# Performance work log

Measured on AMD Instinct MI355X. Metric: run time of the kernel, lower is better.

Reference implementation:

```python
import jax, jax.numpy as jnp
import numpy as np

N, E = 50000, 200000          # nodes, edges
S, V = 256, 128               # 256x0e scalars, 128x1o vectors -> node dim 640
EDGE_DIM, HID = 64, 256
NUM_ATOM, NUM_BOND = 16, 5
FAN_TP = S * S + V * V        # fully-connected TP fan-in for rescale


def setup_inputs() -> dict:
    key = jax.random.key(0)
    ks = jax.random.split(key, 12)
    h_final = jax.random.normal(ks[0], (N, S + 3 * V), dtype=jnp.float32)
    e_final = jax.random.normal(ks[1], (E, EDGE_DIM), dtype=jnp.float32)
    target_node_mask = jnp.ones((N,), dtype=bool)
    target_edge_mask = jnp.ones((E,), dtype=bool)
    edge_index = jax.random.randint(ks[2], (2, E), 0, N)

    def lin(k, o, i):
        return (jax.random.normal(k, (o, i), jnp.float32) / np.sqrt(i)).astype(jnp.float32)

    return {
        "h_final": h_final,
        "e_final": e_final,
        "target_node_mask": target_node_mask,
        "target_edge_mask": target_edge_mask,
        "edge_index": edge_index,
        "Ws_w": lin(ks[3], S, S),          # LinearRS on scalar irreps (with bias)
        "Ws_b": jnp.zeros((S,), jnp.float32),
        "Wv": lin(ks[4], V, V),            # LinearRS on 1o irreps (no bias)
        "Wcoord": (jax.random.normal(ks[5], (V,), jnp.float32) / np.sqrt(V)),  # 128x1o -> 1x1o
        "W_tp00": jax.random.normal(ks[6], (S, S), jnp.float32),  # 0e x 0e -> 0e path weights
        "W_tp11": jax.random.normal(ks[7], (V, V), jnp.float32),  # 1o x 1o -> 0e path weights
        "atom_W1": lin(ks[8], HID, S), "atom_b1": jnp.zeros((HID,), jnp.float32),
        "atom_W2": lin(ks[9], NUM_ATOM, HID), "atom_b2": jnp.zeros((NUM_ATOM,), jnp.float32),
        "bond_W1": lin(ks[10], HID, 1 + EDGE_DIM), "bond_b1": jnp.zeros((HID,), jnp.float32),
        "bond_W2": lin(ks[11], NUM_BOND, HID), "bond_b2": jnp.zeros((NUM_BOND,), jnp.float32),
    }


def reference(h_final, e_final, target_node_mask, target_edge_mask, edge_index,
              Ws_w, Ws_b, Wv, Wcoord, W_tp00, W_tp11,
              atom_W1, atom_b1, atom_W2, atom_b2,
              bond_W1, bond_b1, bond_W2, bond_b2):
    # --- node heads (masks are all-True here; boolean gather kept for faithfulness) ---
    x = h_final[target_node_mask]                 # [Nt, 640]
    xs = x[:, :S]                                 # scalar (0e) part [Nt, 256]
    xv = x[:, S:].reshape(-1, V, 3)               # vector (1o) part [Nt, 128, 3]

    scalar_feats = xs @ Ws_w.T + Ws_b             # node_scalar_proj (LinearRS)
    atom_type_logits = jax.nn.silu(scalar_feats @ atom_W1.T + atom_b1) @ atom_W2.T + atom_b2

    vec = jnp.einsum('nci,dc->ndi', xv, Wv)       # node_vector_proj, per-component channel mix
    predicted_r0 = jnp.einsum('nci,c->ni', vec, Wcoord)  # coord_head -> [Nt, 3]

    # --- bond head: edge gather + fully-connected tensor product to 0e ---
    ei = edge_index[:, target_edge_mask]
    row, col = ei[0], ei[1]
    hr, hc = h_final[row], h_final[col]           # [Et, 640] each
    sr, sc = hr[:, :S], hc[:, :S]
    vr = hr[:, S:].reshape(-1, V, 3)
    vc = hc[:, S:].reshape(-1, V, 3)
    # paths: 0e(x)0e->0e and 1o(x)1o->0e (dot product, CG norm 1/sqrt(3)), rescaled by fan-in
    tp = (jnp.einsum('ei,ej,ij->e', sr, sc, W_tp00)
          + jnp.einsum('eci,edi,cd->e', vr, vc, W_tp11) / np.sqrt(3.0)) / np.sqrt(FAN_TP)
    bond_in = jnp.concatenate([tp[:, None], e_final[target_edge_mask]], axis=-1)  # [Et, 65]
    bond_logits = jax.nn.silu(bond_in @ bond_W1.T + bond_b1) @ bond_W2.T + bond_b2

    return atom_type_logits, predicted_r0, bond_logits
```

## Files before the change

kernel.cpp:

```cpp
#include <hip/hip_runtime.h>

typedef unsigned short u16;
typedef unsigned int u32;
typedef float f32x4 __attribute__((ext_vector_type(4)));
typedef float f32x2 __attribute__((ext_vector_type(2)));
typedef short s16x8 __attribute__((ext_vector_type(8)));
typedef __bf16 bf16x8 __attribute__((ext_vector_type(8)));

#define NNODE 50000
#define NEDGE 200000
#define INV_SQRT3 0.57735026918962576f
#define INV_SQRT_FAN 0.0034938562148434216f

__device__ inline float b2f(u16 x) {
    unsigned u = ((unsigned)x) << 16;
    return __builtin_bit_cast(float, u);
}
__device__ inline u16 f2b(float f) {
    unsigned u = __builtin_bit_cast(unsigned, f);
    unsigned r = u + 0x7FFFu + ((u >> 16) & 1u);
    return (u16)(r >> 16);
}
__device__ inline float silu(float v) { return v / (1.f + __expf(-v)); }

__device__ inline float ld1(const void* p, long i, int m) {
    return m ? ((const float*)p)[i] : b2f(((const u16*)p)[i]);
}
__device__ inline void stout(void* o, long i, float v, int m) {
    if (m) ((float*)o)[i] = v; else ((u16*)o)[i] = f2b(v);
}

#if defined(__has_builtin)
# if __has_builtin(__builtin_amdgcn_cvt_pk_f32_fp8) && __has_builtin(__builtin_amdgcn_cvt_pk_fp8_f32)
#  define HAVE_FP8 1
# endif
#endif
#ifndef HAVE_FP8
# define HAVE_FP8 0
#endif

__device__ inline int f2e4m3_soft(float f) {
    unsigned u = __builtin_bit_cast(unsigned, f);
    int s = (u >> 24) & 0x80;
    float a = __builtin_fabsf(f);
    if (a >= 464.f) return s | 0x7E;
    if (a < 0.015625f) {
        int q = (int)(a * 512.f + 0.5f);
        return s | q;
    }
    int e = (int)((u >> 23) & 0xFF) - 127;
    unsigned m = u & 0x7FFFFF;
    unsigned mq = (m + 0x80000) >> 20;
    if (mq == 8) { mq = 0; e += 1; }
    if (e > 8) return s | 0x7E;
    return s | ((e + 7) << 3) | (int)mq;
}
__device__ inline float e4m3f_soft(int b) {
    int em = b & 0x7F;
    float v;
    if (em >> 3) {
        unsigned bits = ((unsigned)((em >> 3) + 120) << 23) | ((unsigned)(em & 7) << 20);
        v = __builtin_bit_cast(float, bits);
    } else {
        v = (float)em * 0.001953125f;
    }
    return (b & 0x80) ? -v : v;
}
__device__ inline int enc2(float a, float b) {
#if HAVE_FP8
    return __builtin_amdgcn_cvt_pk_fp8_f32(a, b, 0, false) & 0xFFFF;
#else
    return f2e4m3_soft(a) | (f2e4m3_soft(b) << 8);
#endif
}
__device__ inline unsigned char enc1(float a) { return (unsigned char)(enc2(a, a) & 0xFF); }

__device__ inline float dot8(unsigned p, unsigned x, float acc) {
#if HAVE_FP8
    f32x2 p0 = __builtin_amdgcn_cvt_pk_f32_fp8((int)p, false);
    f32x2 p1 = __builtin_amdgcn_cvt_pk_f32_fp8((int)p, true);
    f32x2 x0 = __builtin_amdgcn_cvt_pk_f32_fp8((int)x, false);
    f32x2 x1 = __builtin_amdgcn_cvt_pk_f32_fp8((int)x, true);
    return acc + p0.x * x0.x + p0.y * x0.y + p1.x * x1.x + p1.y * x1.y;
#else
    float r = acc;
#pragma unroll
    for (int i = 0; i < 4; ++i)
        r += e4m3f_soft((p >> (8 * i)) & 0xFF) * e4m3f_soft((x >> (8 * i)) & 0xFF);
    return r;
#endif
}
__device__ inline float dot2(unsigned p, unsigned x, float acc) {
#if HAVE_FP8
    f32x2 p0 = __builtin_amdgcn_cvt_pk_f32_fp8((int)p, false);
    f32x2 x0 = __builtin_amdgcn_cvt_pk_f32_fp8((int)x, false);
    return acc + p0.x * x0.x + p0.y * x0.y;
#else
    return acc + e4m3f_soft(p & 0xFF) * e4m3f_soft(x & 0xFF)
               + e4m3f_soft((p >> 8) & 0xFF) * e4m3f_soft((x >> 8) & 0xFF);
#endif
}

template <typename V>
__device__ auto mfma_sel(V a, V b, f32x4 c, int)
    -> decltype(__builtin_amdgcn_mfma_f32_16x16x32_bf16(a, b, c, 0, 0, 0)) {
    return __builtin_amdgcn_mfma_f32_16x16x32_bf16(a, b, c, 0, 0, 0);
}
template <typename V>
__device__ f32x4 mfma_sel(V a, V b, f32x4 c, long) {
    bf16x8 aa = __builtin_bit_cast(bf16x8, a);
    bf16x8 bb = __builtin_bit_cast(bf16x8, b);
    return __builtin_amdgcn_mfma_f32_16x16x32_bf16(aa, bb, c, 0, 0, 0);
}
__device__ inline f32x4 mfma_bf16(s16x8 a, s16x8 b, f32x4 c) {
    return mfma_sel(a, b, c, 0);
}

typedef __attribute__((address_space(1))) u32 AS1u32;
typedef __attribute__((address_space(3))) u32 AS3u32;
__device__ __forceinline__ void async16(const void* g, void* l) {
    __builtin_amdgcn_global_load_lds((AS1u32*)g, (AS3u32*)l, 16, 0, 0);
}

__global__ __launch_bounds__(256) void detect_k(const void* __restrict__ h, int* __restrict__ flag) {
    int t = threadIdx.x;
    u16 w = ((const u16*)h)[2 * t];
    int tb = (w >> 8) & 0x7F;
    bool pl = (tb >= 0x38 && tb <= 0x41);
    unsigned long long b = __ballot(pl);
    __shared__ int cnt[4];
    if ((t & 63) == 0) cnt[t >> 6] = __popcll(b);
    __syncthreads();
    if (t == 0) {
        int s = cnt[0] + cnt[1] + cnt[2] + cnt[3];
        flag[0] = (s < 128) ? 1 : 0;
    }
}

__global__ __launch_bounds__(256) void prep_misc_k(
    const void* __restrict__ W00, const void* __restrict__ W11,
    const void* __restrict__ bW1, const void* __restrict__ Wv,
    const void* __restrict__ Wcoord, const void* __restrict__ aW2,
    const void* __restrict__ bW2,
    u16* __restrict__ W00T, u16* __restrict__ W1p, u16* __restrict__ W2p,
    float* __restrict__ w1tp, float* __restrict__ w_eff,
    u16* __restrict__ W2ah, u16* __restrict__ W11T,
    const int* __restrict__ mflag)
{
    const int m = *mflag;
    int u = blockIdx.x * 256 + threadIdx.x;
    if (u < 65536) {
        int j = u >> 8, i = u & 255;
        W00T[u] = f2b(ld1(W00, (long)i * 256 + j, m));
    } else if (u < 81920) {
        int v = u - 65536;
        int j = v & 7, ln = (v >> 3) & 63, tk = v >> 9;
        int tn = tk >> 1, kt = tk & 1;
        int hrow = tn * 16 + (ln & 15);
        int k = kt * 32 + (ln >> 4) * 8 + j;
        W1p[v] = f2b(ld1(bW1, (long)hrow * 65 + 1 + k, m));
    } else if (u < 86016) {
        int v = u - 81920;
        int j = v & 7, ln = (v >> 3) & 63, kt = v >> 9;
        int o = ln & 15;
        int k = kt * 32 + (ln >> 4) * 8 + j;
        W2p[v] = (o < 5) ? f2b(ld1(bW2, (long)o * 256 + k, m)) : (u16)0;
    } else if (u < 86272) {
        int hd = u - 86016;
        w1tp[hd] = ld1(bW1, (long)hd * 65, m);
    } else if (u < 86400) {
        int c = u - 86272;
        float acc = 0.f;
        for (int d = 0; d < 128; ++d)
            acc += ld1(Wcoord, d, m) * ld1(Wv, (long)d * 128 + c, m);
        w_eff[c] = acc;
    } else if (u < 90496) {
        int v = u - 86400;
        W2ah[v] = f2b(ld1(aW2, v, m));
    } else if (u < 106880) {
        int v = u - 90496;
        int d = v >> 7, c = v & 127;
        W11T[v] = f2b(ld1(W11, (long)c * 128 + d, m));
    }
}

__global__ __launch_bounds__(256) void prep_w1s_k(
    const void* __restrict__ aW1, const void* __restrict__ Wsw,
    const void* __restrict__ Wsb, const void* __restrict__ ab1,
    u16* __restrict__ W1sh, float* __restrict__ b1p,
    const int* __restrict__ mflag)
{
    const int m = *mflag;
    int hd = blockIdx.x, s = threadIdx.x;
    float acc = 0.f;
    for (int j = 0; j < 256; ++j)
        acc += ld1(aW1, (long)hd * 256 + j, m) * ld1(Wsw, (long)j * 256 + s, m);
    W1sh[hd * 256 + s] = f2b(acc);
    if (s == 0) {
        float b = ld1(ab1, hd, m);
        for (int j = 0; j < 256; ++j)
            b += ld1(aW1, (long)hd * 256 + j, m) * ld1(Wsb, j, m);
        b1p[hd] = b;
    }
}

__device__ __forceinline__ void gemm_core_128(
    const void* __restrict__ Aptr, int lda, int a_f32,
    const u16* __restrict__ Bt, int ldb, int bcol0,
    long bm0, int K, u16* __restrict__ S, f32x4 acc[4][4])
{
    u16* As = S;
    u16* Bs = S + 8192;
    int tid = threadIdx.x;
    int lane = tid & 63, wave = tid >> 6;
    int sr = lane >> 2, sc = (lane & 3) * 8;

    auto stage = [&](int buf, int k0) {
#pragma unroll
        for (int i = 0; i < 2; ++i) {
            int row = wave * 32 + i * 16 + sr;
            async16(Bt + (long)(bcol0 + row) * ldb + k0 + sc,
                    Bs + buf * 4096 + wave * 1024 + i * 512);
        }
        if (!a_f32) {
#pragma unroll
            for (int i = 0; i < 2; ++i) {
                int row = wave * 32 + i * 16 + sr;
                long grow = bm0 + row; if (grow >= NNODE) grow = NNODE - 1;
                async16((const u16*)Aptr + grow * (long)lda + k0 + sc,
                        As + buf * 4096 + wave * 1024 + i * 512);
            }
        } else {
            int r = tid >> 2, c = (tid & 3) * 8;
#pragma unroll
            for (int p = 0; p < 2; ++p) {
                int row = p * 64 + r;
                long grow = bm0 + row; if (grow >= NNODE) grow = NNODE - 1;
                const float* ap = (const float*)Aptr + grow * (long)lda + k0 + c;
                float4 a0 = *(const float4*)ap;
                float4 a1 = *(const float4*)(ap + 4);
                u16 t[8] = {f2b(a0.x), f2b(a0.y), f2b(a0.z), f2b(a0.w),
                            f2b(a1.x), f2b(a1.y), f2b(a1.z), f2b(a1.w)};
                *(ushort4*)(As + buf * 4096 + row * 32 + c)     = *(const ushort4*)&t[0];
                *(ushort4*)(As + buf * 4096 + row * 32 + c + 4) = *(const ushort4*)&t[4];
            }
        }
    };

    int NT = K >> 5;
    stage(0, 0);
    __syncthreads();
    int wm = (wave & 1) * 64, wn = (wave >> 1) * 64;
    int lm = lane & 15, quad = lane >> 4;
    for (int t = 0; t < NT; ++t) {
        int cur = t & 1;
        if (t + 1 < NT) stage(cur ^ 1, (t + 1) * 32);
        const u16* Ac = As + cur * 4096;
        const u16* Bc = Bs + cur * 4096;
        s16x8 af[4], bfr[4];
#pragma unroll
        for (int q = 0; q < 4; ++q) {
            af[q]  = *(const s16x8*)(Ac + (wm + q * 16 + lm) * 32 + quad * 8);
            bfr[q] = *(const s16x8*)(Bc + (wn + q * 16 + lm) * 32 + quad * 8);
        }
#pragma unroll
        for (int i = 0; i < 4; ++i)
#pragma unroll
            for (int j = 0; j < 4; ++j)
                acc[i][j] = mfma_bf16(af[i], bfr[j], acc[i][j]);
        __syncthreads();
    }
}

__global__ __launch_bounds__(256) void mlp1_k(
    const void* __restrict__ A, const u16* __restrict__ Bh,
    const float* __restrict__ b1p, u16* __restrict__ hid,
    const int* __restrict__ mflag)
{
    __shared__ __align__(16) u16 S[16384];
    int bid = blockIdx.x;
    int x = bid & 7, s = bid >> 3;
    int rb = (s >> 1) * 8 + x, cb = s & 1;
    if (rb >= 391) return;
    const int m = *mflag;
    long bm0 = (long)rb * 128;
    int bn0 = cb * 128;
    f32x4 acc[4][4] = {};
    gemm_core_128(A, 640, m, Bh, 256, bn0, bm0, 256, S, acc);

    int tid = threadIdx.x, lane = tid & 63, wave = tid >> 6;
    int wm = (wave & 1) * 64, wn = (wave >> 1) * 64;
    int lm = lane & 15, quad = lane >> 4;
#pragma unroll
    for (int j = 0; j < 4; ++j) {
        int col = wn + j * 16 + lm;
        float bb = b1p[bn0 + col];
#pragma unroll
        for (int i = 0; i < 4; ++i)
#pragma unroll
            for (int rr = 0; rr < 4; ++rr) {
                int row = wm + i * 16 + quad * 4 + rr;
                S[row * 128 + col] = f2b(silu(acc[i][j][rr] + bb));
            }
    }
    __syncthreads();
#pragma unroll
    for (int v = 0; v < 8; ++v) {
        int idx = v * 256 + tid;
        int row = idx >> 4, seg = idx & 15;
        long grow = bm0 + row;
        if (grow < NNODE)
            *(uint4*)(hid + grow * 256 + bn0 + seg * 8) =
                *(const uint4*)(S + row * 128 + seg * 8);
    }
}

__global__ __launch_bounds__(256) void mlp_l2_k(
    const u16* __restrict__ hid, const u16* __restrict__ W2h,
    const void* __restrict__ b2v, void* __restrict__ out,
    const int* __restrict__ mflag)
{
    const int m = *mflag;
    int tid = threadIdx.x, lane = tid & 63, w = tid >> 6;
    int lm = lane & 15, quad = lane >> 4;
    int m0 = blockIdx.x * 64 + w * 16;
    int arow = m0 + lm; if (arow >= NNODE) arow = NNODE - 1;
    const u16* ap = hid + (long)arow * 256;
    const u16* wp = W2h + (long)lm * 256;
    f32x4 acc = {0.f, 0.f, 0.f, 0.f};
#pragma unroll
    for (int k0 = 0; k0 < 256; k0 += 32) {
        s16x8 a  = *(const s16x8*)(ap + k0 + quad * 8);
        s16x8 bh = *(const s16x8*)(wp + k0 + quad * 8);
        acc = mfma_bf16(a, bh, acc);
    }
    float b2 = ld1(b2v, lm, m);
#pragma unroll
    for (int rr = 0; rr < 4; ++rr) {
        int grow = m0 + quad * 4 + rr;
        if (grow < NNODE)
            stout(out, (long)grow * 16 + lm, acc[rr] + b2, m);
    }
}

__global__ __launch_bounds__(256) void packx8_k(
    const void* __restrict__ h, u16* __restrict__ xvp,
    const float* __restrict__ w_eff, unsigned char* __restrict__ X8,
    void* __restrict__ out, const int* __restrict__ mflag)
{
    const int m = *mflag;
    int lane = threadIdx.x & 63, w = threadIdx.x >> 6;
    int node = blockIdx.x * 4 + w;
    if (node >= NNODE) return;
    float s4[4];
    if (m) {
        float4 v = *(const float4*)((const float*)h + (long)node * 640 + lane * 4);
        s4[0] = v.x; s4[1] = v.y; s4[2] = v.z; s4[3] = v.w;
    } else {
        ushort4 v = *(const ushort4*)((const u16*)h + (long)node * 640 + lane * 4);
        s4[0] = b2f(v.x); s4[1] = b2f(v.y); s4[2] = b2f(v.z); s4[3] = b2f(v.w);
    }
    unsigned sp = (unsigned)enc2(s4[0], s4[1]) | ((unsigned)enc2(s4[2], s4[3]) << 16);
    *(unsigned*)(X8 + (long)node * 640 + lane * 4) = sp;
    float a[6];
    if (m) {
        const float* p = (const float*)h + (long)node * 640 + 256 + lane * 6;
        float2 v0 = *(const float2*)p;
        float2 v1 = *(const float2*)(p + 2);
        float2 v2 = *(const float2*)(p + 4);
        a[0] = v0.x; a[1] = v0.y; a[2] = v1.x; a[3] = v1.y; a[4] = v2.x; a[5] = v2.y;
    } else {
        const u16* p = (const u16*)h + (long)node * 640 + 256 + lane * 6;
        ushort2 v0 = *(const ushort2*)p;
        ushort2 v1 = *(const ushort2*)(p + 2);
        ushort2 v2 = *(const ushort2*)(p + 4);
        a[0] = b2f(v0.x); a[1] = b2f(v0.y); a[2] = b2f(v1.x);
        a[3] = b2f(v1.y); a[4] = b2f(v2.x); a[5] = b2f(v2.y);
    }
#pragma unroll
    for (int z = 0; z < 3; ++z) {
        unsigned pk = (unsigned)f2b(a[z]) | ((unsigned)f2b(a[z + 3]) << 16);
        *(unsigned*)(xvp + (long)z * 6400000 + (long)node * 128 + lane * 2) = pk;
        *(unsigned short*)(X8 + (long)node * 640 + 256 + z * 128 + lane * 2) =
            (unsigned short)enc2(a[z], a[z + 3]);
    }
    float2 we = *(const float2*)(w_eff + lane * 2);
    float s0 = a[0] * we.x + a[3] * we.y;
    float s1 = a[1] * we.x + a[4] * we.y;
    float s2 = a[2] * we.x + a[5] * we.y;
#pragma unroll
    for (int off = 32; off > 0; off >>= 1) {
        s0 += __shfl_down(s0, off);
        s1 += __shfl_down(s1, off);
        s2 += __shfl_down(s2, off);
    }
    if (lane == 0) {
        stout(out, 800000L + (long)node * 3 + 0, s0, m);
        stout(out, 800000L + (long)node * 3 + 1, s1, m);
        stout(out, 800000L + (long)node * 3 + 2, s2, m);
    }
}

__global__ __launch_bounds__(256) void gemm8n_k(
    const void* __restrict__ h, const u16* __restrict__ xvp,
    const u16* __restrict__ W00T, const u16* __restrict__ W11T,
    unsigned char* __restrict__ PQ8,
    float s00, float s11, const int* __restrict__ mflag)
{
    __shared__ __align__(16) u16 S[16384];
    int bid = blockIdx.x;
    int x = bid & 7, s = bid >> 3;
    int rb = (s / 5) * 8 + x, cb = s % 5;
    if (rb >= 391) return;
    const int m = *mflag;
    const bool qp = (cb >= 2);
    int z = cb - 2;
    long bm0 = (long)rb * 128;
    f32x4 acc[4][4] = {};
    if (qp)
        gemm_core_128(xvp + (long)z * 6400000, 128, 0, W11T, 128, 0, bm0, 128, S, acc);
    else
        gemm_core_128(h, 640, m, W00T, 256, cb * 128, bm0, 256, S, acc);

    float scale = qp ? s11 : s00;
    int colbase = qp ? (256 + z * 128) : cb * 128;
    unsigned char* C8 = (unsigned char*)S;
    int tid = threadIdx.x, lane = tid & 63, wave = tid >> 6;
    int wm = (wave & 1) * 64, wn = (wave >> 1) * 64;
    int lm = lane & 15, quad = lane >> 4;
#pragma unroll
    for (int j = 0; j < 4; ++j) {
        int col = wn + j * 16 + lm;
#pragma unroll
        for (int i = 0; i < 4; ++i)
#pragma unroll
            for (int rr = 0; rr < 4; ++rr) {
                int row = wm + i * 16 + quad * 4 + rr;
                C8[row * 128 + col] = enc1(scale * acc[i][j][rr]);
            }
    }
    __syncthreads();
#pragma unroll
    for (int v = 0; v < 4; ++v) {
        int idx = v * 256 + tid;
        int row = idx >> 3, seg = idx & 7;
        long grow = bm0 + row;
        if (grow < NNODE)
            *(uint4*)(PQ8 + grow * 640 + colbase + seg * 16) =
                *(const uint4*)(C8 + row * 128 + seg * 16);
    }
}

__global__ __launch_bounds__(256) void bond_fused_k(
    const void* __restrict__ A, const u16* __restrict__ W1p,
    const void* __restrict__ b1v, const u16* __restrict__ W2p,
    const void* __restrict__ b2v, const float* __restrict__ tp,
    const float* __restrict__ w1tp, void* __restrict__ out, long obase,
    const int* __restrict__ mflag)
{
    const int m = *mflag;
    __shared__ __align__(16) u16 hidS[4][16][264];
    int tid = threadIdx.x, lane = tid & 63, w = tid >> 6;
    int lm = lane & 15, quad = lane >> 4;
    int e0 = (blockIdx.x * 4 + w) * 16;
    s16x8 af0, af1;
    long base = (long)(e0 + lm) * 64 + quad * 8;
    if (m) {
        const float* ap = (const float*)A + base;
        float4 a0 = *(const float4*)ap,        a1 = *(const float4*)(ap + 4);
        float4 a2 = *(const float4*)(ap + 32), a3 = *(const float4*)(ap + 36);
        u16 t0[8] = {f2b(a0.x), f2b(a0.y), f2b(a0.z), f2b(a0.w),
                     f2b(a1.x), f2b(a1.y), f2b(a1.z), f2b(a1.w)};
        u16 t1[8] = {f2b(a2.x), f2b(a2.y), f2b(a2.z), f2b(a2.w),
                     f2b(a3.x), f2b(a3.y), f2b(a3.z), f2b(a3.w)};
        af0 = *(const s16x8*)t0; af1 = *(const s16x8*)t1;
    } else {
        af0 = *(const s16x8*)((const u16*)A + base);
        af1 = *(const s16x8*)((const u16*)A + base + 32);
    }
    float4 tpv = *(const float4*)(tp + e0 + quad * 4);
    float tpr[4] = {tpv.x, tpv.y, tpv.z, tpv.w};
    f32x4 acc1[16];
#pragma unroll
    for (int tn = 0; tn < 16; ++tn) {
        s16x8 b0 = *(const s16x8*)(W1p + ((tn * 2 + 0) * 64 + lane) * 8);
        s16x8 b1f = *(const s16x8*)(W1p + ((tn * 2 + 1) * 64 + lane) * 8);
        f32x4 a = {0.f, 0.f, 0.f, 0.f};
        a = mfma_bf16(af0, b0, a);
        a = mfma_bf16(af1, b1f, a);
        acc1[tn] = a;
    }
#pragma unroll
    for (int tn = 0; tn < 16; ++tn) {
        int hcol = tn * 16 + lm;
        float bb = ld1(b1v, hcol, m);
        float wt = w1tp[hcol];
#pragma unroll
        for (int rr = 0; rr < 4; ++rr)
            hidS[w][quad * 4 + rr][hcol] = f2b(silu(acc1[tn][rr] + bb + tpr[rr] * wt));
    }
    f32x4 acc2 = {0.f, 0.f, 0.f, 0.f};
#pragma unroll
    for (int kt = 0; kt < 8; ++kt) {
        s16x8 a = *(const s16x8*)&hidS[w][lm][kt * 32 + quad * 8];
        s16x8 b = *(const s16x8*)(W2p + (kt * 64 + lane) * 8);
        acc2 = mfma_bf16(a, b, acc2);
    }
    if (lm < 5) {
        float b2 = ld1(b2v, lm, m);
#pragma unroll
        for (int rr = 0; rr < 4; ++rr) {
            int e = e0 + quad * 4 + rr;
            stout(out, obase + (long)e * 5 + lm, acc2[rr] + b2, m);
        }
    }
}

__global__ __launch_bounds__(256) void tp_k(
    const int* __restrict__ ei, const unsigned char* __restrict__ PQ8,
    const unsigned char* __restrict__ X8, float* __restrict__ tp)
{
    int wave = threadIdx.x >> 6, lane = threadIdx.x & 63;
    int e = blockIdx.x * 4 + wave;
    if (e >= NEDGE) return;
    int row = ei[e], col = ei[NEDGE + e];
    const unsigned char* pq = PQ8 + (long)row * 640;
    const unsigned char* xp = X8 + (long)col * 640;
    uint2 pw = *(const uint2*)(pq + lane * 8);
    uint2 xw = *(const uint2*)(xp + lane * 8);
    unsigned pt = *(const unsigned short*)(pq + 512 + lane * 2);
    unsigned xt = *(const unsigned short*)(xp + 512 + lane * 2);
    float acc = 0.f;
    acc = dot8(pw.x, xw.x, acc);
    acc = dot8(pw.y, xw.y, acc);
    acc = dot2(pt, xt, acc);
#pragma unroll
    for (int off = 32; off > 0; off >>= 1) acc += __shfl_down(acc, off);
    if (lane == 0) tp[e] = acc * 0.0625f;
}

extern "C" void kernel_launch(void* const* d_in, const int* in_sizes, int n_in,
                              void* d_out, int out_size, void* d_ws, size_t ws_size,
                              hipStream_t stream) {
    (void)in_sizes; (void)n_in; (void)out_size; (void)ws_size;
    const void* h      = d_in[0];
    const void* e_fin  = d_in[1];
    const int*  ei     = (const int*)d_in[4];
    const void* Ws_w   = d_in[5];
    const void* Ws_b   = d_in[6];
    const void* Wv     = d_in[7];
    const void* Wcoord = d_in[8];
    const void* W00    = d_in[9];
    const void* W11    = d_in[10];
    const void* aW1    = d_in[11];
    const void* ab1    = d_in[12];
    const void* aW2    = d_in[13];
    const void* ab2    = d_in[14];
    const void* bW1    = d_in[15];
    const void* bb1    = d_in[16];
    const void* bW2    = d_in[17];
    const void* bb2    = d_in[18];

    char* ws = (char*)d_ws;
    int*   mflag = (int*)(ws + 0);
    float* w1tp  = (float*)(ws + 512);
    float* w_eff = (float*)(ws + 2048);
    float* b1p   = (float*)(ws + 3072);
    u16*   W00T  = (u16*)(ws + 4096);
    u16*   W1p   = (u16*)(ws + 135168);
    u16*   W2p   = (u16*)(ws + 167936);
    u16*   W1sh  = (u16*)(ws + 176128);
    u16*   W2ah  = (u16*)(ws + 307200);
    u16*   W11T  = (u16*)(ws + 315392);
    float* tp    = (float*)(ws + 348160);
    char*  R     = ws + 1149184;
    unsigned char* PQ8  = (unsigned char*)R;
    unsigned char* X8   = (unsigned char*)(R + 33554432);
    u16*           hidA = (u16*)(R + 67108864);
    u16*           xvp  = (u16*)(R + 67108864);

    detect_k<<<1, 256, 0, stream>>>(h, mflag);
    prep_misc_k<<<418, 256, 0, stream>>>(W00, W11, bW1, Wv, Wcoord, aW2, bW2,
                                         W00T, W1p, W2p, w1tp, w_eff,
                                         W2ah, W11T, mflag);
    prep_w1s_k<<<256, 256, 0, stream>>>(aW1, Ws_w, Ws_b, ab1, W1sh, b1p, mflag);

    mlp1_k<<<784, 256, 0, stream>>>(h, W1sh, b1p, hidA, mflag);
    mlp_l2_k<<<782, 256, 0, stream>>>(hidA, W2ah, ab2, d_out, mflag);

    packx8_k<<<12500, 256, 0, stream>>>(h, xvp, w_eff, X8, d_out, mflag);

    gemm8n_k<<<1960, 256, 0, stream>>>(h, xvp, W00T, W11T, PQ8,
                                       16.f * INV_SQRT_FAN,
                                       16.f * INV_SQRT_FAN * INV_SQRT3, mflag);
    tp_k<<<50000, 256, 0, stream>>>(ei, PQ8, X8, tp);

    bond_fused_k<<<3125, 256, 0, stream>>>(e_fin, W1p, bb1, W2p, bb2,
                                           tp, w1tp, d_out, 950000L, mflag);
}
```

Before: 501.2 us.

## Fuse atom MLP second layer into first, pre-pack bf16 scalars, narrow tp_k lanes

The atom head's second linear layer now runs inside mlp1_k on the hidden tile held in shared memory. Its partial results from the two column blocks are combined with atomicAdd into a zeroed fp32 buffer, and a small finalize kernel adds the bias. This removes the bf16 hidden-activation round trip through global memory. packx8_k now also writes a bf16 copy of the scalar features, so both GEMMs load bf16 through async copies instead of converting fp32 on the fly. tp_k is changed to use 16 lanes per edge with 16-byte loads instead of a full wave per edge. The cost is an extra zeroing kernel, atomic traffic, and a larger workspace.

```diff
diff --git a/kernel.cpp b/kernel.cpp
--- a/kernel.cpp
+++ b/kernel.cpp
@@ -88,16 +88,6 @@
     for (int i = 0; i < 4; ++i)
         r += e4m3f_soft((p >> (8 * i)) & 0xFF) * e4m3f_soft((x >> (8 * i)) & 0xFF);
     return r;
-#endif
-}
-__device__ inline float dot2(unsigned p, unsigned x, float acc) {
-#if HAVE_FP8
-    f32x2 p0 = __builtin_amdgcn_cvt_pk_f32_fp8((int)p, false);
-    f32x2 x0 = __builtin_amdgcn_cvt_pk_f32_fp8((int)x, false);
-    return acc + p0.x * x0.x + p0.y * x0.y;
-#else
-    return acc + e4m3f_soft(p & 0xFF) * e4m3f_soft(x & 0xFF)
-               + e4m3f_soft((p >> 8) & 0xFF) * e4m3f_soft((x >> 8) & 0xFF);
 #endif
 }
 
@@ -204,8 +194,13 @@
     }
 }
 
+__global__ __launch_bounds__(256) void zero_k(float4* __restrict__ p) {
+    int t = blockIdx.x * 256 + threadIdx.x;
+    if (t < 200000) p[t] = float4{0.f, 0.f, 0.f, 0.f};
+}
+
 __device__ __forceinline__ void gemm_core_128(
-    const void* __restrict__ Aptr, int lda, int a_f32,
+    const u16* __restrict__ Aptr, int lda,
     const u16* __restrict__ Bt, int ldb, int bcol0,
     long bm0, int K, u16* __restrict__ S, f32x4 acc[4][4])
 {
@@ -221,29 +216,9 @@
             int row = wave * 32 + i * 16 + sr;
             async16(Bt + (long)(bcol0 + row) * ldb + k0 + sc,
                     Bs + buf * 4096 + wave * 1024 + i * 512);
-        }
-        if (!a_f32) {
-#pragma unroll
-            for (int i = 0; i < 2; ++i) {
-                int row = wave * 32 + i * 16 + sr;
-                long grow = bm0 + row; if (grow >= NNODE) grow = NNODE - 1;
-                async16((const u16*)Aptr + grow * (long)lda + k0 + sc,
-                        As + buf * 4096 + wave * 1024 + i * 512);
-            }
-        } else {
-            int r = tid >> 2, c = (tid & 3) * 8;
-#pragma unroll
-            for (int p = 0; p < 2; ++p) {
-                int row = p * 64 + r;
-                long grow = bm0 + row; if (grow >= NNODE) grow = NNODE - 1;
-                const float* ap = (const float*)Aptr + grow * (long)lda + k0 + c;
-                float4 a0 = *(const float4*)ap;
-                float4 a1 = *(const float4*)(ap + 4);
-                u16 t[8] = {f2b(a0.x), f2b(a0.y), f2b(a0.z), f2b(a0.w),
-                            f2b(a1.x), f2b(a1.y), f2b(a1.z), f2b(a1.w)};
-                *(ushort4*)(As + buf * 4096 + row * 32 + c)     = *(const ushort4*)&t[0];
-                *(ushort4*)(As + buf * 4096 + row * 32 + c + 4) = *(const ushort4*)&t[4];
-            }
+            long grow = bm0 + row; if (grow >= NNODE) grow = NNODE - 1;
+            async16(Aptr + grow * (long)lda + k0 + sc,
+                    As + buf * 4096 + wave * 1024 + i * 512);
         }
     };
 
@@ -273,20 +248,19 @@
 }
 
 __global__ __launch_bounds__(256) void mlp1_k(
-    const void* __restrict__ A, const u16* __restrict__ Bh,
-    const float* __restrict__ b1p, u16* __restrict__ hid,
-    const int* __restrict__ mflag)
-{
-    __shared__ __align__(16) u16 S[16384];
+    const u16* __restrict__ Xs16, const u16* __restrict__ Bh,
+    const float* __restrict__ b1p, const u16* __restrict__ W2ah,
+    float* __restrict__ outP)
+{
+    __shared__ __align__(16) u16 S[17408];
     int bid = blockIdx.x;
     int x = bid & 7, s = bid >> 3;
     int rb = (s >> 1) * 8 + x, cb = s & 1;
     if (rb >= 391) return;
-    const int m = *mflag;
     long bm0 = (long)rb * 128;
     int bn0 = cb * 128;
     f32x4 acc[4][4] = {};
-    gemm_core_128(A, 640, m, Bh, 256, bn0, bm0, 256, S, acc);
+    gemm_core_128(Xs16, 256, Bh, 256, bn0, bm0, 256, S, acc);
 
     int tid = threadIdx.x, lane = tid & 63, wave = tid >> 6;
     int wm = (wave & 1) * 64, wn = (wave >> 1) * 64;
@@ -298,55 +272,44 @@
 #pragma unroll
         for (int i = 0; i < 4; ++i)
 #pragma unroll
-            for (int rr = 0; rr < 4; ++rr) {
-                int row = wm + i * 16 + quad * 4 + rr;
-                S[row * 128 + col] = f2b(silu(acc[i][j][rr] + bb));
-            }
+            for (int rr = 0; rr < 4; ++rr)
+                S[(wm + i * 16 + quad * 4 + rr) * 136 + col] = f2b(silu(acc[i][j][rr] + bb));
     }
     __syncthreads();
-#pragma unroll
-    for (int v = 0; v < 8; ++v) {
-        int idx = v * 256 + tid;
-        int row = idx >> 4, seg = idx & 15;
-        long grow = bm0 + row;
-        if (grow < NNODE)
-            *(uint4*)(hid + grow * 256 + bn0 + seg * 8) =
-                *(const uint4*)(S + row * 128 + seg * 8);
-    }
-}
-
-__global__ __launch_bounds__(256) void mlp_l2_k(
-    const u16* __restrict__ hid, const u16* __restrict__ W2h,
-    const void* __restrict__ b2v, void* __restrict__ out,
-    const int* __restrict__ mflag)
+    const u16* wp = W2ah + lm * 256 + bn0;
+#pragma unroll
+    for (int rg = 0; rg < 2; ++rg) {
+        int r0 = wave * 32 + rg * 16;
+        f32x4 a2 = {0.f, 0.f, 0.f, 0.f};
+#pragma unroll
+        for (int k0 = 0; k0 < 128; k0 += 32) {
+            s16x8 a = *(const s16x8*)(S + (r0 + lm) * 136 + k0 + quad * 8);
+            s16x8 b = *(const s16x8*)(wp + k0 + quad * 8);
+            a2 = mfma_bf16(a, b, a2);
+        }
+#pragma unroll
+        for (int rr = 0; rr < 4; ++rr) {
+            long grow = bm0 + r0 + quad * 4 + rr;
+            if (grow < NNODE)
+                atomicAdd(outP + grow * 16 + lm, a2[rr]);
+        }
+    }
+}
+
+__global__ __launch_bounds__(256) void fin_atom_k(
+    const float* __restrict__ outP, const void* __restrict__ b2v,
+    void* __restrict__ out, const int* __restrict__ mflag)
 {
     const int m = *mflag;
-    int tid = threadIdx.x, lane = tid & 63, w = tid >> 6;
-    int lm = lane & 15, quad = lane >> 4;
-    int m0 = blockIdx.x * 64 + w * 16;
-    int arow = m0 + lm; if (arow >= NNODE) arow = NNODE - 1;
-    const u16* ap = hid + (long)arow * 256;
-    const u16* wp = W2h + (long)lm * 256;
-    f32x4 acc = {0.f, 0.f, 0.f, 0.f};
-#pragma unroll
-    for (int k0 = 0; k0 < 256; k0 += 32) {
-        s16x8 a  = *(const s16x8*)(ap + k0 + quad * 8);
-        s16x8 bh = *(const s16x8*)(wp + k0 + quad * 8);
-        acc = mfma_bf16(a, bh, acc);
-    }
-    float b2 = ld1(b2v, lm, m);
-#pragma unroll
-    for (int rr = 0; rr < 4; ++rr) {
-        int grow = m0 + quad * 4 + rr;
-        if (grow < NNODE)
-            stout(out, (long)grow * 16 + lm, acc[rr] + b2, m);
-    }
+    int t = blockIdx.x * 256 + threadIdx.x;
+    stout(out, t, outP[t] + ld1(b2v, t & 15, m), m);
 }
 
 __global__ __launch_bounds__(256) void packx8_k(
     const void* __restrict__ h, u16* __restrict__ xvp,
     const float* __restrict__ w_eff, unsigned char* __restrict__ X8,
-    void* __restrict__ out, const int* __restrict__ mflag)
+    u16* __restrict__ Xs16, void* __restrict__ out,
+    const int* __restrict__ mflag)
 {
     const int m = *mflag;
     int lane = threadIdx.x & 63, w = threadIdx.x >> 6;
@@ -362,6 +325,8 @@
     }
     unsigned sp = (unsigned)enc2(s4[0], s4[1]) | ((unsigned)enc2(s4[2], s4[3]) << 16);
     *(unsigned*)(X8 + (long)node * 640 + lane * 4) = sp;
+    u16 sx[4] = {f2b(s4[0]), f2b(s4[1]), f2b(s4[2]), f2b(s4[3])};
+    *(ushort4*)(Xs16 + (long)node * 256 + lane * 4) = *(const ushort4*)sx;
     float a[6];
     if (m) {
         const float* p = (const float*)h + (long)node * 640 + 256 + lane * 6;
@@ -402,25 +367,23 @@
 }
 
 __global__ __launch_bounds__(256) void gemm8n_k(
-    const void* __restrict__ h, const u16* __restrict__ xvp,
+    const u16* __restrict__ Xs16, const u16* __restrict__ xvp,
     const u16* __restrict__ W00T, const u16* __restrict__ W11T,
-    unsigned char* __restrict__ PQ8,
-    float s00, float s11, const int* __restrict__ mflag)
+    unsigned char* __restrict__ PQ8, float s00, float s11)
 {
     __shared__ __align__(16) u16 S[16384];
     int bid = blockIdx.x;
     int x = bid & 7, s = bid >> 3;
     int rb = (s / 5) * 8 + x, cb = s % 5;
     if (rb >= 391) return;
-    const int m = *mflag;
     const bool qp = (cb >= 2);
     int z = cb - 2;
     long bm0 = (long)rb * 128;
     f32x4 acc[4][4] = {};
     if (qp)
-        gemm_core_128(xvp + (long)z * 6400000, 128, 0, W11T, 128, 0, bm0, 128, S, acc);
+        gemm_core_128(xvp + (long)z * 6400000, 128, W11T, 128, 0, bm0, 128, S, acc);
     else
-        gemm_core_128(h, 640, m, W00T, 256, cb * 128, bm0, 256, S, acc);
+        gemm_core_128(Xs16, 256, W00T, 256, cb * 128, bm0, 256, S, acc);
 
     float scale = qp ? s11 : s00;
     int colbase = qp ? (256 + z * 128) : cb * 128;
@@ -520,23 +483,28 @@
     const int* __restrict__ ei, const unsigned char* __restrict__ PQ8,
     const unsigned char* __restrict__ X8, float* __restrict__ tp)
 {
-    int wave = threadIdx.x >> 6, lane = threadIdx.x & 63;
-    int e = blockIdx.x * 4 + wave;
+    int tid = threadIdx.x;
+    int sub = tid & 15;
+    int e = blockIdx.x * 16 + (tid >> 4);
     if (e >= NEDGE) return;
     int row = ei[e], col = ei[NEDGE + e];
     const unsigned char* pq = PQ8 + (long)row * 640;
     const unsigned char* xp = X8 + (long)col * 640;
-    uint2 pw = *(const uint2*)(pq + lane * 8);
-    uint2 xw = *(const uint2*)(xp + lane * 8);
-    unsigned pt = *(const unsigned short*)(pq + 512 + lane * 2);
-    unsigned xt = *(const unsigned short*)(xp + 512 + lane * 2);
+    uint4 p0 = *(const uint4*)(pq + sub * 16);
+    uint4 x0 = *(const uint4*)(xp + sub * 16);
+    uint4 p1 = *(const uint4*)(pq + 256 + sub * 16);
+    uint4 x1 = *(const uint4*)(xp + 256 + sub * 16);
+    uint2 p2 = *(const uint2*)(pq + 512 + sub * 8);
+    uint2 x2 = *(const uint2*)(xp + 512 + sub * 8);
     float acc = 0.f;
-    acc = dot8(pw.x, xw.x, acc);
-    acc = dot8(pw.y, xw.y, acc);
-    acc = dot2(pt, xt, acc);
-#pragma unroll
-    for (int off = 32; off > 0; off >>= 1) acc += __shfl_down(acc, off);
-    if (lane == 0) tp[e] = acc * 0.0625f;
+    acc = dot8(p0.x, x0.x, acc); acc = dot8(p0.y, x0.y, acc);
+    acc = dot8(p0.z, x0.z, acc); acc = dot8(p0.w, x0.w, acc);
+    acc = dot8(p1.x, x1.x, acc); acc = dot8(p1.y, x1.y, acc);
+    acc = dot8(p1.z, x1.z, acc); acc = dot8(p1.w, x1.w, acc);
+    acc = dot8(p2.x, x2.x, acc); acc = dot8(p2.y, x2.y, acc);
+#pragma unroll
+    for (int off = 8; off > 0; off >>= 1) acc += __shfl_down(acc, off);
+    if (sub == 0) tp[e] = acc * 0.0625f;
 }
 
 extern "C" void kernel_launch(void* const* d_in, const int* in_sizes, int n_in,
@@ -576,24 +544,26 @@
     char*  R     = ws + 1149184;
     unsigned char* PQ8  = (unsigned char*)R;
     unsigned char* X8   = (unsigned char*)(R + 33554432);
-    u16*           hidA = (u16*)(R + 67108864);
     u16*           xvp  = (u16*)(R + 67108864);
+    u16*           Xs16 = (u16*)(R + 105906176);
+    float*         outP = (float*)(R + 132120576);
 
     detect_k<<<1, 256, 0, stream>>>(h, mflag);
     prep_misc_k<<<418, 256, 0, stream>>>(W00, W11, bW1, Wv, Wcoord, aW2, bW2,
                                          W00T, W1p, W2p, w1tp, w_eff,
                                          W2ah, W11T, mflag);
     prep_w1s_k<<<256, 256, 0, stream>>>(aW1, Ws_w, Ws_b, ab1, W1sh, b1p, mflag);
-
-    mlp1_k<<<784, 256, 0, stream>>>(h, W1sh, b1p, hidA, mflag);
-    mlp_l2_k<<<782, 256, 0, stream>>>(hidA, W2ah, ab2, d_out, mflag);
-
-    packx8_k<<<12500, 256, 0, stream>>>(h, xvp, w_eff, X8, d_out, mflag);
-
-    gemm8n_k<<<1960, 256, 0, stream>>>(h, xvp, W00T, W11T, PQ8,
+    zero_k<<<782, 256, 0, stream>>>((float4*)outP);
+
+    packx8_k<<<12500, 256, 0, stream>>>(h, xvp, w_eff, X8, Xs16, d_out, mflag);
+
+    mlp1_k<<<784, 256, 0, stream>>>(Xs16, W1sh, b1p, W2ah, outP);
+    fin_atom_k<<<3125, 256, 0, stream>>>(outP, ab2, d_out, mflag);
+
+    gemm8n_k<<<1960, 256, 0, stream>>>(Xs16, xvp, W00T, W11T, PQ8,
                                        16.f * INV_SQRT_FAN,
-                                       16.f * INV_SQRT_FAN * INV_SQRT3, mflag);
-    tp_k<<<50000, 256, 0, stream>>>(ei, PQ8, X8, tp);
+                                       16.f * INV_SQRT_FAN * INV_SQRT3);
+    tp_k<<<12500, 256, 0, stream>>>(ei, PQ8, X8, tp);
 
     bond_fused_k<<<3125, 256, 0, stream>>>(e_fin, W1p, bb1, W2p, bb2,
                                            tp, w1tp, d_out, 950000L, mflag);
```

Result: faster. 483.4 us (-3.5%).
